# Performance work log

Measured on AMD Instinct MI355X. Metric: run time of the kernel, lower is better.

The kernel has to match this reference:

```python
import jax, jax.numpy as jnp
import numpy as np

D_EMB = 512
N_HEADS = 8
D_K = 64
D_V = 64
D_FF = 2048
N_LAYERS = 6
VOCAB = 32000
SRC_LEN = 512


def sin_enc_table(n_position, d):
    pos = jnp.arange(n_position, dtype=jnp.float32)[:, None]
    j = jnp.arange(d, dtype=jnp.float32)[None, :]
    angle = pos / jnp.power(10000.0, 2.0 * jnp.floor(j / 2.0) / d)
    return jnp.where((jnp.arange(d) % 2 == 0)[None, :], jnp.sin(angle), jnp.cos(angle))


def layer_norm(x, gamma, beta, eps=1e-5):
    mu = jnp.mean(x, axis=-1, keepdims=True)
    var = jnp.mean(jnp.square(x - mu), axis=-1, keepdims=True)
    return (x - mu) * jax.lax.rsqrt(var + eps) * gamma + beta


def setup_inputs() -> dict:
    key = jax.random.key(0)
    ks = jax.random.split(key, 20)
    s = 0.02
    L = N_LAYERS
    inp = {
        'enc_inputs': jax.random.randint(ks[0], (16, 512), 0, VOCAB),
        'emb': jax.random.normal(ks[1], (VOCAB, D_EMB), jnp.float32) * s,
        'Wq': jax.random.normal(ks[2], (L, N_HEADS * D_K, D_EMB), jnp.float32) * s,
        'bq': jnp.zeros((L, N_HEADS * D_K), jnp.float32),
        'Wk': jax.random.normal(ks[3], (L, N_HEADS * D_K, D_EMB), jnp.float32) * s,
        'bk': jnp.zeros((L, N_HEADS * D_K), jnp.float32),
        'Wv': jax.random.normal(ks[4], (L, N_HEADS * D_V, D_EMB), jnp.float32) * s,
        'bv': jnp.zeros((L, N_HEADS * D_V), jnp.float32),
        'Wo': jax.random.normal(ks[5], (L, D_EMB, N_HEADS * D_V), jnp.float32) * s,
        'bo': jnp.zeros((L, D_EMB), jnp.float32),
        'g1': jnp.ones((L, D_EMB), jnp.float32),
        'b1': jnp.zeros((L, D_EMB), jnp.float32),
        'Wc1': jax.random.normal(ks[6], (L, D_FF, D_EMB), jnp.float32) * s,
        'bc1': jnp.zeros((L, D_FF), jnp.float32),
        'Wc2': jax.random.normal(ks[7], (L, D_EMB, D_FF), jnp.float32) * s,
        'bc2': jnp.zeros((L, D_EMB), jnp.float32),
        'g2': jnp.ones((L, D_EMB), jnp.float32),
        'b2': jnp.zeros((L, D_EMB), jnp.float32),
    }
    return inp


def encoder_fwd(enc_inputs, emb, Wq, bq, Wk, bk, Wv, bv, Wo, bo, g1, b1, Wc1, bc1, Wc2, bc2, g2, b2):
    B, S = enc_inputs.shape
    pos_table = sin_enc_table(SRC_LEN + 1, D_EMB)  # frozen
    x = emb[enc_inputs] + pos_table[jnp.arange(1, S + 1)][None, :, :]
    # pad mask: True where key token == 0; broadcast over heads and queries
    pad = (enc_inputs == 0)[:, None, None, :]  # [B,1,1,S]
    scale = 1.0 / np.sqrt(D_K)
    attn_weights = []
    for l in range(N_LAYERS):
        residual = x
        q = (x @ Wq[l].T + bq[l]).reshape(B, S, N_HEADS, D_K).transpose(0, 2, 1, 3)
        k = (x @ Wk[l].T + bk[l]).reshape(B, S, N_HEADS, D_K).transpose(0, 2, 1, 3)
        v = (x @ Wv[l].T + bv[l]).reshape(B, S, N_HEADS, D_V).transpose(0, 2, 1, 3)
        scores = jnp.einsum('bhqd,bhkd->bhqk', q, k) * scale
        scores = jnp.where(pad, -1e9, scores)
        w = jax.nn.softmax(scores, axis=-1)
        ctx = jnp.einsum('bhqk,bhkd->bhqd', w, v)
        ctx = ctx.transpose(0, 2, 1, 3).reshape(B, S, N_HEADS * D_V)
        x = layer_norm(ctx @ Wo[l].T + bo[l] + residual, g1[l], b1[l])
        # position-wise FFN (conv1d k=1 == dense)
        h = jax.nn.relu(x @ Wc1[l].T + bc1[l])
        x = layer_norm(h @ Wc2[l].T + bc2[l] + x, g2[l], b2[l])
        attn_weights.append(w)
    return x, jnp.stack(attn_weights)


def reference(enc_inputs, emb, Wq, bq, Wk, bk, Wv, bv, Wo, bo, g1, b1, Wc1, bc1, Wc2, bc2, g2, b2):
    return encoder_fwd(enc_inputs, emb, Wq, bq, Wk, bk, Wv, bv, Wo, bo, g1, b1, Wc1, bc1, Wc2, bc2, g2, b2)
```

## Files before the change

### kernel.cpp

```cpp
#include <hip/hip_runtime.h>

typedef unsigned short u16;
typedef __attribute__((ext_vector_type(8))) short s16x8;
typedef __attribute__((ext_vector_type(4))) float f32x4;
typedef __attribute__((ext_vector_type(4))) unsigned short u16x4;

#define DEVI __device__ __forceinline__

DEVI float bf2f(u16 h) { union { unsigned u; float f; } v; v.u = ((unsigned)h) << 16; return v.f; }
DEVI u16 f2bf(float f) {
  union { unsigned u; float f; } v; v.f = f;
  unsigned u = v.u;
  unsigned r = (u + 0x7fffu + ((u >> 16) & 1u)) >> 16;
  return (u16)r;
}

DEVI f32x4 mfma16(s16x8 a, s16x8 b, f32x4 c) {
  return __builtin_amdgcn_mfma_f32_16x16x32_bf16(a, b, c, 0, 0, 0);
}

DEVI void cvt8(const float* __restrict__ in, u16* __restrict__ out, int i) {
  const f32x4* p = (const f32x4*)(in + (size_t)i * 8);
  f32x4 a = p[0], b = p[1];
  u16x4 o0 = { f2bf(a[0]), f2bf(a[1]), f2bf(a[2]), f2bf(a[3]) };
  u16x4 o1 = { f2bf(b[0]), f2bf(b[1]), f2bf(b[2]), f2bf(b[3]) };
  u16x4* q = (u16x4*)(out + (size_t)i * 8);
  q[0] = o0; q[1] = o1;
}

__global__ void prep_kern(const float* __restrict__ Wq, const float* __restrict__ Wk,
                          const float* __restrict__ Wv, const float* __restrict__ Wo,
                          const float* __restrict__ Wc1, const float* __restrict__ Wc2,
                          const float* __restrict__ bq, const float* __restrict__ bk,
                          const float* __restrict__ bv,
                          u16* __restrict__ Wqkvb, u16* __restrict__ Wob,
                          u16* __restrict__ Wc1b, u16* __restrict__ Wc2b,
                          float* __restrict__ bqkvb) {
  const int Rqkv = 6 * 1536 * 512 / 8;
  const int Rwo  = 6 * 512 * 512 / 8;
  const int Rw1  = 6 * 2048 * 512 / 8;
  const int Rw2  = Rw1;
  const int Rb   = 6 * 1536 / 8;
  const int total = Rqkv + Rwo + Rw1 + Rw2 + Rb;
  for (int idx = blockIdx.x * blockDim.x + threadIdx.x; idx < total;
       idx += gridDim.x * blockDim.x) {
    int i = idx;
    if (i < Rqkv) {
      int c8 = i & 63;
      int t = i >> 6;
      int r = t % 1536, l = t / 1536;
      const float* src; int rr = r;
      if (r < 512) src = Wq;
      else if (r < 1024) { src = Wk; rr = r - 512; }
      else { src = Wv; rr = r - 1024; }
      const f32x4* p = (const f32x4*)(src + ((size_t)(l * 512 + rr) * 512) + c8 * 8);
      f32x4 a = p[0], b = p[1];
      u16x4 o0 = { f2bf(a[0]), f2bf(a[1]), f2bf(a[2]), f2bf(a[3]) };
      u16x4 o1 = { f2bf(b[0]), f2bf(b[1]), f2bf(b[2]), f2bf(b[3]) };
      u16x4* q = (u16x4*)(Wqkvb + (size_t)i * 8);
      q[0] = o0; q[1] = o1;
      continue;
    }
    i -= Rqkv;
    if (i < Rwo) { cvt8(Wo, Wob, i); continue; }
    i -= Rwo;
    if (i < Rw1) { cvt8(Wc1, Wc1b, i); continue; }
    i -= Rw1;
    if (i < Rw2) { cvt8(Wc2, Wc2b, i); continue; }
    i -= Rw2;
    #pragma unroll
    for (int u = 0; u < 8; ++u) {
      int j = i * 8 + u;
      int l = j / 1536, r = j % 1536;
      float v = (r < 512) ? bq[l * 512 + r]
              : (r < 1024) ? bk[l * 512 + r - 512] : bv[l * 512 + r - 1024];
      bqkvb[j] = v;
    }
  }
}

__global__ void embed_kern(const int* __restrict__ tok, const float* __restrict__ emb,
                           u16* __restrict__ xb) {
  int bs = blockIdx.x;
  int s = bs & 511;
  int t = threadIdx.x;
  int id = tok[bs];
  float pos = (float)(s + 1);
  int j0 = t * 4;
  f32x4 e = *(const f32x4*)(emb + (size_t)id * 512 + j0);
  u16x4 ob;
  #pragma unroll
  for (int u = 0; u < 4; ++u) {
    int j = j0 + u;
    float expo = (float)(j & ~1) * (1.0f / 512.0f);
    float ang = pos / powf(10000.0f, expo);
    float pe = (j & 1) ? cosf(ang) : sinf(ang);
    ob[u] = f2bf(e[u] + pe);
  }
  *(u16x4*)(xb + (size_t)bs * 512 + j0) = ob;
}

template <int WM, bool RELU>
__global__ __launch_bounds__(256, 2) void gemm_bs(const u16* __restrict__ A,
                                                  const u16* __restrict__ Bt,
                                                  const float* __restrict__ bias,
                                                  u16* __restrict__ Cb,
                                                  int N, int K, int nN) {
  constexpr int MF = WM / 16;
  constexpr int RPB = WM * 4;
  __shared__ __align__(16) u16 Bsw[128 * 256];

  const int chunkw = gridDim.x >> 3;
  const int wgid = (blockIdx.x & 7) * chunkw + (blockIdx.x >> 3);
  const int n = wgid % nN, m = wgid / nN;
  const int bn0 = n * 128, bm0 = m * RPB;

  const int tid = threadIdx.x, lane = tid & 63, wid = tid >> 6;
  const int l15 = lane & 15, lhi = lane >> 4;
  const int mrow0 = bm0 + wid * WM;

  f32x4 acc[MF][8];
  #pragma unroll
  for (int i = 0; i < MF; ++i)
    #pragma unroll
    for (int j = 0; j < 8; ++j)
      #pragma unroll
      for (int r = 0; r < 4; ++r) acc[i][j][r] = 0.0f;

  const u16* aB[MF];
  #pragma unroll
  for (int i = 0; i < MF; ++i)
    aB[i] = A + (size_t)(mrow0 + i * 16 + l15) * K + lhi * 8;

  const int rounds = K >> 8;
  for (int r = 0; r < rounds; ++r) {
    const int kb = r << 8;
    s16x8 tmp[16];
    #pragma unroll
    for (int c = 0; c < 16; ++c) {
      int cc = c * 256 + tid;
      int row = cc >> 5, col = cc & 31;
      tmp[c] = *(const s16x8*)(Bt + (size_t)(bn0 + row) * K + kb + col * 8);
    }
    __syncthreads();
    #pragma unroll
    for (int c = 0; c < 16; ++c) {
      int cc = c * 256 + tid;
      int row = cc >> 5, col = cc & 31;
      int byte = row * 512 + ((col * 16) ^ ((row & 7) << 4));
      *(s16x8*)((char*)Bsw + byte) = tmp[c];
    }
    __syncthreads();
    #pragma unroll
    for (int ks = 0; ks < 8; ++ks) {
      s16x8 af[MF], bf[8];
      #pragma unroll
      for (int i = 0; i < MF; ++i)
        af[i] = *(const s16x8*)(aB[i] + kb + ks * 32);
      #pragma unroll
      for (int j = 0; j < 8; ++j) {
        int row = j * 16 + l15;
        int byte = row * 512 + (((ks * 64) + lhi * 16) ^ ((row & 7) << 4));
        bf[j] = *(const s16x8*)((char*)Bsw + byte);
      }
      #pragma unroll
      for (int i = 0; i < MF; ++i)
        #pragma unroll
        for (int j = 0; j < 8; ++j)
          acc[i][j] = mfma16(af[i], bf[j], acc[i][j]);
    }
  }

  const int r0 = mrow0 + lhi * 4;
  const int c0 = bn0 + l15;
  #pragma unroll
  for (int i = 0; i < MF; ++i)
    #pragma unroll
    for (int j = 0; j < 8; ++j) {
      int col = c0 + j * 16;
      float bv = bias[col];
      #pragma unroll
      for (int r = 0; r < 4; ++r) {
        int row = r0 + i * 16 + r;
        float v = acc[i][j][r] + bv;
        if (RELU) v = fmaxf(v, 0.0f);
        Cb[(size_t)row * N + col] = f2bf(v);
      }
    }
}

__global__ void ln2_kern(const u16* __restrict__ parts,
                         const u16* __restrict__ resid,
                         const float* __restrict__ gam, const float* __restrict__ bet,
                         float* __restrict__ outf, u16* __restrict__ outb) {
  int row = blockIdx.x * 4 + (threadIdx.x >> 6);
  int t = threadIdx.x & 63;
  size_t base = (size_t)row * 512;
  const u16x4* pp = (const u16x4*)(parts + base);
  u16x4 pa = pp[t], pb4 = pp[t + 64];
  const u16x4* rp = (const u16x4*)(resid + base);
  u16x4 ra = rp[t], rb = rp[t + 64];
  f32x4 v0, v1;
  #pragma unroll
  for (int u = 0; u < 4; ++u) {
    v0[u] = bf2f(pa[u]) + bf2f(ra[u]);
    v1[u] = bf2f(pb4[u]) + bf2f(rb[u]);
  }

  float s = v0[0] + v0[1] + v0[2] + v0[3] + v1[0] + v1[1] + v1[2] + v1[3];
  float q = v0[0]*v0[0] + v0[1]*v0[1] + v0[2]*v0[2] + v0[3]*v0[3]
          + v1[0]*v1[0] + v1[1]*v1[1] + v1[2]*v1[2] + v1[3]*v1[3];
  #pragma unroll
  for (int d = 1; d < 64; d <<= 1) { s += __shfl_xor(s, d, 64); q += __shfl_xor(q, d, 64); }
  float mu = s * (1.0f / 512.0f);
  float var = q * (1.0f / 512.0f) - mu * mu;
  float rs = rsqrtf(var + 1e-5f);
  const f32x4* gp = (const f32x4*)gam;
  const f32x4* bp = (const f32x4*)bet;
  f32x4 ga = gp[t], gb = gp[t + 64], ba = bp[t], bb = bp[t + 64];
  f32x4 o0, o1; u16x4 ob0, ob1;
  #pragma unroll
  for (int u = 0; u < 4; ++u) {
    float a0 = (v0[u] - mu) * rs * ga[u] + ba[u];
    float a1 = (v1[u] - mu) * rs * gb[u] + bb[u];
    o0[u] = a0; o1[u] = a1; ob0[u] = f2bf(a0); ob1[u] = f2bf(a1);
  }
  u16x4* obp = (u16x4*)(outb + base);
  obp[t] = ob0; obp[t + 64] = ob1;
  if (outf) {
    f32x4* op = (f32x4*)(outf + base);
    op[t] = o0; op[t + 64] = o1;
  }
}

__global__ void vtrans_kern(const u16* __restrict__ QKV, u16* __restrict__ Vt) {
  int bx = blockIdx.x;
  int st = bx & 7, h = (bx >> 3) & 7, b = bx >> 6;
  int s0 = st * 64;
  __shared__ __align__(16) u16 tile[64][72];
  int t = threadIdx.x;
  for (int c = t; c < 512; c += 256) {
    int r = c >> 3, cc = (c & 7) << 3;
    *(s16x8*)&tile[r][cc] =
        *(const s16x8*)&QKV[(size_t)(b * 512 + s0 + r) * 1536 + 1024 + h * 64 + cc];
  }
  __syncthreads();
  for (int c = t; c < 512; c += 256) {
    int d = c >> 3, sc = (c & 7) << 3;
    s16x8 o;
    #pragma unroll
    for (int i2 = 0; i2 < 8; ++i2) o[i2] = (short)tile[sc + i2][d];
    *(s16x8*)&Vt[((size_t)(b * 8 + h) * 64 + d) * 512 + s0 + sc] = o;
  }
}

__global__ void attn_kern(const u16* __restrict__ QKV, const u16* __restrict__ Vt,
                          const int* __restrict__ tok,
                          float* __restrict__ wout, u16* __restrict__ ctxb) {
  int wg = (blockIdx.x & 7) * 256 + (blockIdx.x >> 3);
  int qt = wg & 15;
  int h = (wg >> 4) & 7;
  int b = wg >> 7;
  int tid = threadIdx.x;
  int lane = tid & 63, wid = tid >> 6;
  int l15 = lane & 15, lhi = lane >> 4;
  int m0 = qt * 32;

  __shared__ __align__(16) u16 Wl[32][528];
  __shared__ float pmask[512];
  __shared__ float redbuf[2][32][4];

  for (int c = tid; c < 512; c += 256)
    pmask[c] = (tok[b * 512 + c] == 0) ? 1.0f : 0.0f;

  s16x8 qf[2][2];
  const u16* qbase = QKV + (size_t)(b * 512 + m0) * 1536 + h * 64;
  #pragma unroll
  for (int i = 0; i < 2; ++i)
    #pragma unroll
    for (int kk = 0; kk < 2; ++kk)
      qf[i][kk] = *(const s16x8*)(qbase + (size_t)(i * 16 + l15) * 1536 + kk * 32 + lhi * 8);

  f32x4 sacc[2][8];
  #pragma unroll
  for (int i = 0; i < 2; ++i)
    #pragma unroll
    for (int j = 0; j < 8; ++j)
      #pragma unroll
      for (int r = 0; r < 4; ++r) sacc[i][j][r] = 0.0f;

  int c0 = wid * 128;
  const u16* kbase = QKV + (size_t)(b * 512 + c0) * 1536 + 512 + h * 64;
  #pragma unroll
  for (int j = 0; j < 8; ++j) {
    #pragma unroll
    for (int kk = 0; kk < 2; ++kk) {
      s16x8 kf = *(const s16x8*)(kbase + (size_t)(j * 16 + l15) * 1536 + kk * 32 + lhi * 8);
      sacc[0][j] = mfma16(qf[0][kk], kf, sacc[0][j]);
      sacc[1][j] = mfma16(qf[1][kk], kf, sacc[1][j]);
    }
  }
  __syncthreads();

  float rm[2][4], sm[2][4], gi[2][4];
  #pragma unroll
  for (int i = 0; i < 2; ++i)
    #pragma unroll
    for (int r = 0; r < 4; ++r) rm[i][r] = -3.0e38f;

  #pragma unroll
  for (int j = 0; j < 8; ++j) {
    float pm = pmask[c0 + j * 16 + l15];
    #pragma unroll
    for (int i = 0; i < 2; ++i)
      #pragma unroll
      for (int r = 0; r < 4; ++r) {
        float sv = sacc[i][j][r] * 0.125f;
        sv = (pm != 0.0f) ? -1.0e9f : sv;
        sacc[i][j][r] = sv;
        rm[i][r] = fmaxf(rm[i][r], sv);
      }
  }
  #pragma unroll
  for (int d = 1; d < 16; d <<= 1)
    #pragma unroll
    for (int i = 0; i < 2; ++i)
      #pragma unroll
      for (int r = 0; r < 4; ++r)
        rm[i][r] = fmaxf(rm[i][r], __shfl_xor(rm[i][r], d, 64));

  if (l15 == 0) {
    #pragma unroll
    for (int i = 0; i < 2; ++i)
      #pragma unroll
      for (int r = 0; r < 4; ++r)
        redbuf[0][i * 16 + lhi * 4 + r][wid] = rm[i][r];
  }
  __syncthreads();
  #pragma unroll
  for (int i = 0; i < 2; ++i)
    #pragma unroll
    for (int r = 0; r < 4; ++r) {
      int row = i * 16 + lhi * 4 + r;
      rm[i][r] = fmaxf(fmaxf(redbuf[0][row][0], redbuf[0][row][1]),
                       fmaxf(redbuf[0][row][2], redbuf[0][row][3]));
      sm[i][r] = 0.0f;
    }
  #pragma unroll
  for (int j = 0; j < 8; ++j)
    #pragma unroll
    for (int i = 0; i < 2; ++i)
      #pragma unroll
      for (int r = 0; r < 4; ++r) {
        float pv = __expf(sacc[i][j][r] - rm[i][r]);
        sacc[i][j][r] = pv;
        sm[i][r] += pv;
      }
  #pragma unroll
  for (int d = 1; d < 16; d <<= 1)
    #pragma unroll
    for (int i = 0; i < 2; ++i)
      #pragma unroll
      for (int r = 0; r < 4; ++r)
        sm[i][r] += __shfl_xor(sm[i][r], d, 64);
  if (l15 == 0) {
    #pragma unroll
    for (int i = 0; i < 2; ++i)
      #pragma unroll
      for (int r = 0; r < 4; ++r)
        redbuf[1][i * 16 + lhi * 4 + r][wid] = sm[i][r];
  }
  __syncthreads();
  #pragma unroll
  for (int i = 0; i < 2; ++i)
    #pragma unroll
    for (int r = 0; r < 4; ++r) {
      int row = i * 16 + lhi * 4 + r;
      float tot = redbuf[1][row][0] + redbuf[1][row][1] + redbuf[1][row][2] + redbuf[1][row][3];
      gi[i][r] = 1.0f / tot;
    }

  float* wrow = wout + ((size_t)((b * 8 + h) * 512 + m0)) * 512;
  #pragma unroll
  for (int j = 0; j < 8; ++j)
    #pragma unroll
    for (int i = 0; i < 2; ++i)
      #pragma unroll
      for (int r = 0; r < 4; ++r) {
        float wv = sacc[i][j][r] * gi[i][r];
        int row = i * 16 + lhi * 4 + r;
        int col = c0 + j * 16 + l15;
        Wl[row][col] = f2bf(wv);
        __builtin_nontemporal_store(wv, &wrow[(size_t)row * 512 + col]);
      }
  __syncthreads();

  f32x4 cacc[2];
  #pragma unroll
  for (int i = 0; i < 2; ++i)
    #pragma unroll
    for (int r = 0; r < 4; ++r) cacc[i][r] = 0.0f;
  const u16* vbase = Vt + ((size_t)((b * 8 + h) * 64 + wid * 16 + l15)) * 512;
  #pragma unroll
  for (int kk = 0; kk < 16; ++kk) {
    s16x8 vf = *(const s16x8*)(vbase + kk * 32 + lhi * 8);
    #pragma unroll
    for (int i = 0; i < 2; ++i) {
      s16x8 wf = *(const s16x8*)&Wl[i * 16 + l15][kk * 32 + lhi * 8];
      cacc[i] = mfma16(wf, vf, cacc[i]);
    }
  }

  __syncthreads();
  u16* ct = &Wl[0][0];
  #pragma unroll
  for (int i = 0; i < 2; ++i)
    #pragma unroll
    for (int r = 0; r < 4; ++r)
      ct[(i * 16 + lhi * 4 + r) * 72 + wid * 16 + l15] = f2bf(cacc[i][r]);
  __syncthreads();
  {
    int row = tid >> 3, col = (tid & 7) * 8;
    s16x8 v = *(const s16x8*)&ct[row * 72 + col];
    *(s16x8*)&ctxb[(size_t)(b * 512 + m0 + row) * 512 + h * 64 + col] = v;
  }
}

extern "C" void kernel_launch(void* const* d_in, const int* in_sizes, int n_in,
                              void* d_out, int out_size, void* d_ws, size_t ws_size,
                              hipStream_t stream) {
  const int*   tok = (const int*)d_in[0];
  const float* emb = (const float*)d_in[1];
  const float* Wq  = (const float*)d_in[2];
  const float* bq  = (const float*)d_in[3];
  const float* Wk  = (const float*)d_in[4];
  const float* bk  = (const float*)d_in[5];
  const float* Wv  = (const float*)d_in[6];
  const float* bv  = (const float*)d_in[7];
  const float* Wo  = (const float*)d_in[8];
  const float* bo  = (const float*)d_in[9];
  const float* g1  = (const float*)d_in[10];
  const float* b1  = (const float*)d_in[11];
  const float* Wc1 = (const float*)d_in[12];
  const float* bc1 = (const float*)d_in[13];
  const float* Wc2 = (const float*)d_in[14];
  const float* bc2 = (const float*)d_in[15];
  const float* g2  = (const float*)d_in[16];
  const float* b2  = (const float*)d_in[17];
  (void)in_sizes; (void)n_in; (void)out_size; (void)ws_size;

  float* out_x = (float*)d_out;
  float* out_w = out_x + (size_t)16 * 512 * 512;

  char* p = (char*)d_ws;
  size_t off = 0;
  auto alloc = [&](size_t bytes) { char* r = p + off; off += (bytes + 255) & ~(size_t)255; return r; };
  u16*   xb  = (u16*)alloc((size_t)8192 * 512 * 2);
  u16*   pwo = (u16*)alloc((size_t)8192 * 512 * 2);
  char*  regA = alloc((size_t)8192 * 1536 * 2 + (size_t)8192 * 512 * 2);
  u16* QKVb = (u16*)regA;
  u16* Vtb  = QKVb + (size_t)8192 * 1536;
  u16* hb   = (u16*)regA;
  u16* ctxb = (u16*)alloc((size_t)8192 * 512 * 2);
  u16* Wqkvb = (u16*)alloc((size_t)6 * 1536 * 512 * 2);
  u16* Wob   = (u16*)alloc((size_t)6 * 512 * 512 * 2);
  u16* Wc1b  = (u16*)alloc((size_t)6 * 2048 * 512 * 2);
  u16* Wc2b  = (u16*)alloc((size_t)6 * 2048 * 512 * 2);
  float* bqkvb = (float*)alloc((size_t)6 * 1536 * 4);

  prep_kern<<<2048, 256, 0, stream>>>(Wq, Wk, Wv, Wo, Wc1, Wc2, bq, bk, bv,
                                      Wqkvb, Wob, Wc1b, Wc2b, bqkvb);
  embed_kern<<<8192, 128, 0, stream>>>(tok, emb, xb);

  for (int l = 0; l < 6; ++l) {
    const u16* wqkv_l = Wqkvb + (size_t)l * 1536 * 512;
    const u16* wo_l = Wob + (size_t)l * 512 * 512;
    const u16* w1_l = Wc1b + (size_t)l * 2048 * 512;
    const u16* w2_l = Wc2b + (size_t)l * 2048 * 512;

    gemm_bs<32, false><<<768, 256, 0, stream>>>(xb, wqkv_l, bqkvb + l * 1536,
                                                QKVb, 1536, 512, 12);
    vtrans_kern<<<1024, 256, 0, stream>>>(QKVb, Vtb);
    attn_kern<<<2048, 256, 0, stream>>>(QKVb, Vtb, tok,
                                        out_w + (size_t)l * 8 * 16 * 512 * 512, ctxb);
    gemm_bs<16, false><<<512, 256, 0, stream>>>(ctxb, wo_l, bo + l * 512,
                                                pwo, 512, 512, 4);
    ln2_kern<<<2048, 256, 0, stream>>>(pwo, xb, g1 + l * 512, b1 + l * 512, nullptr, xb);
    gemm_bs<32, true><<<1024, 256, 0, stream>>>(xb, w1_l, bc1 + l * 2048,
                                                hb, 2048, 512, 16);
    gemm_bs<16, false><<<512, 256, 0, stream>>>(hb, w2_l, bc2 + l * 512,
                                                pwo, 512, 2048, 4);
    ln2_kern<<<2048, 256, 0, stream>>>(pwo, xb, g2 + l * 512, b2 + l * 512,
                                       (l == 5 ? out_x : nullptr), xb);
  }
}
```

Baseline: 1.051 ms.

## Fuse V transpose into QKV GEMM epilogue, prefetch B tiles, merge embed into prep

The QKV GEMM epilogue now writes V columns directly in transposed layout through shared memory, so the separate vtrans kernel and its extra pass over V go away. The GEMM main loop also loads the next K-slab of B into registers while MFMAs run on the current slab, so global loads overlap with compute. The embedding kernel is folded into the weight-prep kernel, which saves a launch. Costs are higher register pressure from the prefetch buffer and extra shared-memory traffic and syncs in the V epilogue.

```diff
diff --git a/kernel.cpp b/kernel.cpp
--- a/kernel.cpp
+++ b/kernel.cpp
@@ -33,15 +33,17 @@
                           const float* __restrict__ Wc1, const float* __restrict__ Wc2,
                           const float* __restrict__ bq, const float* __restrict__ bk,
                           const float* __restrict__ bv,
+                          const int* __restrict__ tok, const float* __restrict__ emb,
                           u16* __restrict__ Wqkvb, u16* __restrict__ Wob,
                           u16* __restrict__ Wc1b, u16* __restrict__ Wc2b,
-                          float* __restrict__ bqkvb) {
+                          float* __restrict__ bqkvb, u16* __restrict__ xb) {
   const int Rqkv = 6 * 1536 * 512 / 8;
   const int Rwo  = 6 * 512 * 512 / 8;
   const int Rw1  = 6 * 2048 * 512 / 8;
   const int Rw2  = Rw1;
   const int Rb   = 6 * 1536 / 8;
-  const int total = Rqkv + Rwo + Rw1 + Rw2 + Rb;
+  const int Remb = 8192 * 128;
+  const int total = Rqkv + Rwo + Rw1 + Rw2 + Rb + Remb;
   for (int idx = blockIdx.x * blockDim.x + threadIdx.x; idx < total;
        idx += gridDim.x * blockDim.x) {
     int i = idx;
@@ -68,43 +70,45 @@
     i -= Rw1;
     if (i < Rw2) { cvt8(Wc2, Wc2b, i); continue; }
     i -= Rw2;
-    #pragma unroll
-    for (int u = 0; u < 8; ++u) {
-      int j = i * 8 + u;
-      int l = j / 1536, r = j % 1536;
-      float v = (r < 512) ? bq[l * 512 + r]
-              : (r < 1024) ? bk[l * 512 + r - 512] : bv[l * 512 + r - 1024];
-      bqkvb[j] = v;
-    }
-  }
-}
-
-__global__ void embed_kern(const int* __restrict__ tok, const float* __restrict__ emb,
-                           u16* __restrict__ xb) {
-  int bs = blockIdx.x;
-  int s = bs & 511;
-  int t = threadIdx.x;
-  int id = tok[bs];
-  float pos = (float)(s + 1);
-  int j0 = t * 4;
-  f32x4 e = *(const f32x4*)(emb + (size_t)id * 512 + j0);
-  u16x4 ob;
-  #pragma unroll
-  for (int u = 0; u < 4; ++u) {
-    int j = j0 + u;
-    float expo = (float)(j & ~1) * (1.0f / 512.0f);
-    float ang = pos / powf(10000.0f, expo);
-    float pe = (j & 1) ? cosf(ang) : sinf(ang);
-    ob[u] = f2bf(e[u] + pe);
-  }
-  *(u16x4*)(xb + (size_t)bs * 512 + j0) = ob;
-}
-
-template <int WM, bool RELU>
+    if (i < Rb) {
+      #pragma unroll
+      for (int u = 0; u < 8; ++u) {
+        int j = i * 8 + u;
+        int l = j / 1536, r = j % 1536;
+        float v = (r < 512) ? bq[l * 512 + r]
+                : (r < 1024) ? bk[l * 512 + r - 512] : bv[l * 512 + r - 1024];
+        bqkvb[j] = v;
+      }
+      continue;
+    }
+    i -= Rb;
+    {
+      int bs = i >> 7;
+      int t = i & 127;
+      int s = bs & 511;
+      int id = tok[bs];
+      float pos = (float)(s + 1);
+      int j0 = t * 4;
+      f32x4 e = *(const f32x4*)(emb + (size_t)id * 512 + j0);
+      u16x4 ob;
+      #pragma unroll
+      for (int u = 0; u < 4; ++u) {
+        int j = j0 + u;
+        float expo = (float)(j & ~1) * (1.0f / 512.0f);
+        float ang = pos / powf(10000.0f, expo);
+        float pe = (j & 1) ? cosf(ang) : sinf(ang);
+        ob[u] = f2bf(e[u] + pe);
+      }
+      *(u16x4*)(xb + (size_t)bs * 512 + j0) = ob;
+    }
+  }
+}
+
+template <int WM, bool RELU, bool VT>
 __global__ __launch_bounds__(256, 2) void gemm_bs(const u16* __restrict__ A,
                                                   const u16* __restrict__ Bt,
                                                   const float* __restrict__ bias,
-                                                  u16* __restrict__ Cb,
+                                                  u16* __restrict__ Cb, u16* __restrict__ Vt,
                                                   int N, int K, int nN) {
   constexpr int MF = WM / 16;
   constexpr int RPB = WM * 4;
@@ -132,16 +136,20 @@
   for (int i = 0; i < MF; ++i)
     aB[i] = A + (size_t)(mrow0 + i * 16 + l15) * K + lhi * 8;
 
-  const int rounds = K >> 8;
-  for (int r = 0; r < rounds; ++r) {
-    const int kb = r << 8;
-    s16x8 tmp[16];
+  auto loadB = [&](s16x8* tmp, int kb) {
     #pragma unroll
     for (int c = 0; c < 16; ++c) {
       int cc = c * 256 + tid;
       int row = cc >> 5, col = cc & 31;
       tmp[c] = *(const s16x8*)(Bt + (size_t)(bn0 + row) * K + kb + col * 8);
     }
+  };
+
+  const int rounds = K >> 8;
+  s16x8 tmp[16];
+  loadB(tmp, 0);
+  for (int r = 0; r < rounds; ++r) {
+    const int kb = r << 8;
     __syncthreads();
     #pragma unroll
     for (int c = 0; c < 16; ++c) {
@@ -151,6 +159,7 @@
       *(s16x8*)((char*)Bsw + byte) = tmp[c];
     }
     __syncthreads();
+    if (r + 1 < rounds) loadB(tmp, (r + 1) << 8);
     #pragma unroll
     for (int ks = 0; ks < 8; ++ks) {
       s16x8 af[MF], bf[8];
@@ -173,20 +182,49 @@
 
   const int r0 = mrow0 + lhi * 4;
   const int c0 = bn0 + l15;
-  #pragma unroll
-  for (int i = 0; i < MF; ++i)
-    #pragma unroll
-    for (int j = 0; j < 8; ++j) {
-      int col = c0 + j * 16;
-      float bv = bias[col];
-      #pragma unroll
-      for (int r = 0; r < 4; ++r) {
-        int row = r0 + i * 16 + r;
-        float v = acc[i][j][r] + bv;
-        if (RELU) v = fmaxf(v, 0.0f);
-        Cb[(size_t)row * N + col] = f2bf(v);
-      }
-    }
+  if (VT && bn0 >= 1024) {
+    __syncthreads();
+    u16* T = Bsw;
+    #pragma unroll
+    for (int i = 0; i < MF; ++i)
+      #pragma unroll
+      for (int j = 0; j < 8; ++j) {
+        int col = c0 + j * 16;
+        float bv = bias[col];
+        int lr0 = wid * WM + i * 16 + lhi * 4;
+        int lc = j * 16 + l15;
+        #pragma unroll
+        for (int r = 0; r < 4; ++r)
+          T[(lr0 + r) * 136 + lc] = f2bf(acc[i][j][r] + bv);
+      }
+    __syncthreads();
+    const int b = bm0 >> 9, s0 = bm0 & 511;
+    for (int c = tid; c < 2048; c += 256) {
+      int dr = c >> 4;
+      int ch = c & 15;
+      s16x8 v;
+      #pragma unroll
+      for (int k = 0; k < 8; ++k) v[k] = T[(ch * 8 + k) * 136 + dr];
+      int hc = bn0 - 1024 + dr;
+      int h = hc >> 6, d = hc & 63;
+      *(s16x8*)&Vt[((size_t)((b * 8 + h) * 64 + d)) * 512 + s0 + ch * 8] = v;
+    }
+  } else {
+    #pragma unroll
+    for (int i = 0; i < MF; ++i)
+      #pragma unroll
+      for (int j = 0; j < 8; ++j) {
+        int col = c0 + j * 16;
+        float bv = bias[col];
+        #pragma unroll
+        for (int r = 0; r < 4; ++r) {
+          int row = r0 + i * 16 + r;
+          float v = acc[i][j][r] + bv;
+          if (RELU) v = fmaxf(v, 0.0f);
+          Cb[(size_t)row * N + col] = f2bf(v);
+        }
+      }
+  }
 }
 
 __global__ void ln2_kern(const u16* __restrict__ parts,
@@ -230,27 +268,6 @@
   if (outf) {
     f32x4* op = (f32x4*)(outf + base);
     op[t] = o0; op[t + 64] = o1;
-  }
-}
-
-__global__ void vtrans_kern(const u16* __restrict__ QKV, u16* __restrict__ Vt) {
-  int bx = blockIdx.x;
-  int st = bx & 7, h = (bx >> 3) & 7, b = bx >> 6;
-  int s0 = st * 64;
-  __shared__ __align__(16) u16 tile[64][72];
-  int t = threadIdx.x;
-  for (int c = t; c < 512; c += 256) {
-    int r = c >> 3, cc = (c & 7) << 3;
-    *(s16x8*)&tile[r][cc] =
-        *(const s16x8*)&QKV[(size_t)(b * 512 + s0 + r) * 1536 + 1024 + h * 64 + cc];
-  }
-  __syncthreads();
-  for (int c = t; c < 512; c += 256) {
-    int d = c >> 3, sc = (c & 7) << 3;
-    s16x8 o;
-    #pragma unroll
-    for (int i2 = 0; i2 < 8; ++i2) o[i2] = (short)tile[sc + i2][d];
-    *(s16x8*)&Vt[((size_t)(b * 8 + h) * 64 + d) * 512 + s0 + sc] = o;
   }
 }
 
@@ -468,9 +485,8 @@
   u16* Wc2b  = (u16*)alloc((size_t)6 * 2048 * 512 * 2);
   float* bqkvb = (float*)alloc((size_t)6 * 1536 * 4);
 
-  prep_kern<<<2048, 256, 0, stream>>>(Wq, Wk, Wv, Wo, Wc1, Wc2, bq, bk, bv,
-                                      Wqkvb, Wob, Wc1b, Wc2b, bqkvb);
-  embed_kern<<<8192, 128, 0, stream>>>(tok, emb, xb);
+  prep_kern<<<2048, 256, 0, stream>>>(Wq, Wk, Wv, Wo, Wc1, Wc2, bq, bk, bv, tok, emb,
+                                      Wqkvb, Wob, Wc1b, Wc2b, bqkvb, xb);
 
   for (int l = 0; l < 6; ++l) {
     const u16* wqkv_l = Wqkvb + (size_t)l * 1536 * 512;
@@ -478,18 +494,17 @@
     const u16* w1_l = Wc1b + (size_t)l * 2048 * 512;
     const u16* w2_l = Wc2b + (size_t)l * 2048 * 512;
 
-    gemm_bs<32, false><<<768, 256, 0, stream>>>(xb, wqkv_l, bqkvb + l * 1536,
-                                                QKVb, 1536, 512, 12);
-    vtrans_kern<<<1024, 256, 0, stream>>>(QKVb, Vtb);
+    gemm_bs<32, false, true><<<768, 256, 0, stream>>>(xb, wqkv_l, bqkvb + l * 1536,
+                                                      QKVb, Vtb, 1536, 512, 12);
     attn_kern<<<2048, 256, 0, stream>>>(QKVb, Vtb, tok,
                                         out_w + (size_t)l * 8 * 16 * 512 * 512, ctxb);
-    gemm_bs<16, false><<<512, 256, 0, stream>>>(ctxb, wo_l, bo + l * 512,
-                                                pwo, 512, 512, 4);
+    gemm_bs<16, false, false><<<512, 256, 0, stream>>>(ctxb, wo_l, bo + l * 512,
+                                                       pwo, nullptr, 512, 512, 4);
     ln2_kern<<<2048, 256, 0, stream>>>(pwo, xb, g1 + l * 512, b1 + l * 512, nullptr, xb);
-    gemm_bs<32, true><<<1024, 256, 0, stream>>>(xb, w1_l, bc1 + l * 2048,
-                                                hb, 2048, 512, 16);
-    gemm_bs<16, false><<<512, 256, 0, stream>>>(hb, w2_l, bc2 + l * 512,
-                                                pwo, 512, 2048, 4);
+    gemm_bs<32, true, false><<<1024, 256, 0, stream>>>(xb, w1_l, bc1 + l * 2048,
+                                                       hb, nullptr, 2048, 512, 16);
+    gemm_bs<16, false, false><<<512, 256, 0, stream>>>(hb, w2_l, bc2 + l * 512,
+                                                       pwo, nullptr, 512, 2048, 4);
     ln2_kern<<<2048, 256, 0, stream>>>(pwo, xb, g2 + l * 512, b2 + l * 512,
                                        (l == 5 ? out_x : nullptr), xb);
   }
```

After: 1.077 ms. 2.5% more time.
